# Kernel optimization log

Hardware: AMD Instinct MI355X
Metric: run time of the kernel (lower is better)

## Reference

```python
import jax, jax.numpy as jnp
import numpy as np

MIN_NORM = 1e-15
PROJ_EPS = 4e-3  # HGCN float32 boundary eps
C = 1.0          # curvature (all layers)
N_BRANCH = 4


def artanh(x):
    return jnp.arctanh(jnp.clip(x, -1.0 + 1e-7, 1.0 - 1e-7))


def _norm(x):
    return jnp.clip(jnp.linalg.norm(x, axis=-1, keepdims=True), MIN_NORM)


def proj(x, c):
    n = _norm(x)
    maxn = (1.0 - PROJ_EPS) / jnp.sqrt(c)
    return jnp.where(n > maxn, x / n * maxn, x)


def expmap0(u, c):
    sc = jnp.sqrt(c)
    n = _norm(u)
    return jnp.tanh(sc * n) * u / (sc * n)


def logmap0(p, c):
    sc = jnp.sqrt(c)
    n = _norm(p)
    return artanh(sc * n) * p / (sc * n)


def mobius_add(x, y, c):
    x2 = jnp.sum(x * x, -1, keepdims=True)
    y2 = jnp.sum(y * y, -1, keepdims=True)
    xy = jnp.sum(x * y, -1, keepdims=True)
    num = (1.0 + 2.0 * c * xy + c * y2) * x + (1.0 - c * x2) * y
    den = 1.0 + 2.0 * c * xy + c * c * x2 * y2
    return num / jnp.clip(den, MIN_NORM)


def mobius_matvec(W, x, c):
    sc = jnp.sqrt(c)
    xn = _norm(x)
    mx = x @ W.T
    mxn = _norm(mx)
    res = jnp.tanh(mxn / xn * artanh(sc * xn)) * mx / (mxn * sc)
    zero = jnp.all(mx == 0, axis=-1, keepdims=True)
    return jnp.where(zero, jnp.zeros((), x.dtype), res)


def mobius_mulscaler(r, x, c):
    sc = jnp.sqrt(c)
    xn = _norm(x)
    return jnp.tanh(r * artanh(sc * xn)) * x / (xn * sc)


def spmm(src, dst, w, xt, n):
    # out[i] = sum_{e: dst[e]=i} w[e] * xt[src[e]]
    return jax.ops.segment_sum(w[:, None] * xt[src], dst, num_segments=n)


def hgc_layer(h, W, b, src, dst, w, n):
    # HypLinear (dropout=0)
    h = proj(mobius_matvec(W, h, C), C)
    hb = proj(expmap0(b[None, :], C), C)
    h = proj(mobius_add(h, hb, C), C)
    # HypAgg: sparse propagation in tangent space
    st = spmm(src, dst, w, logmap0(h, C), n)
    h = proj(expmap0(st, C), C)
    # HypAct (relu)
    return proj(expmap0(jax.nn.relu(logmap0(h, C)), C), C)


def encode(x, W0, b0, W1, b1, src, dst, w, n):
    h = proj(expmap0(x, C), C)  # proj_tan0 is identity on Poincare ball
    h = hgc_layer(h, W0, b0, src, dst, w, n)
    h = hgc_layer(h, W1, b1, src, dst, w, n)
    return h


def setup_inputs() -> dict:
    key = jax.random.key(0)
    ks = jax.random.split(key, 8)
    N, F_IN, HID, DIM, E = 50000, 128, 128, 64, 1600000
    x = jax.random.normal(ks[0], (N, F_IN), jnp.float32)
    edge_src = jax.random.randint(ks[1], (E,), 0, N, jnp.int32)
    edge_dst = jax.random.randint(ks[2], (E,), 0, N, jnp.int32)
    # positive, roughly row-normalized edge weights (avg degree 32)
    edge_w = jax.random.uniform(ks[3], (N_BRANCH, E), jnp.float32) / 32.0
    W0 = jax.random.normal(ks[4], (N_BRANCH, HID, F_IN), jnp.float32) * 0.05
    b0 = jax.random.normal(ks[5], (N_BRANCH, HID), jnp.float32) * 0.01
    W1 = jax.random.normal(ks[6], (N_BRANCH, DIM, HID), jnp.float32) * 0.05
    b1 = jax.random.normal(ks[7], (N_BRANCH, DIM), jnp.float32) * 0.01
    return {"x": x, "edge_src": edge_src, "edge_dst": edge_dst, "edge_w": edge_w,
            "W0": W0, "b0": b0, "W1": W1, "b1": b1}


def reference(x, edge_src, edge_dst, edge_w, W0, b0, W1, b1):
    n = x.shape[0]
    # 4 directional-proximity branches (d_i, d_o, n_i, n_o); fixed small loop
    branches = [encode(x, W0[i], b0[i], W1[i], b1[i], edge_src, edge_dst, edge_w[i], n)
                for i in range(N_BRANCH)]
    # Mobius-weighted (scalar 1/8) combination, left-to-right mobius_add chain
    target = mobius_mulscaler(0.125, branches[0], C)
    for br in branches[1:]:
        target = mobius_add(target, mobius_mulscaler(0.125, br, C), C)
    feat = jnp.stack(branches + [target], axis=1)  # [N, 5, dim]
    # HypAttnAgg (use_att=False) with row-normalized per-node star adjacency:
    # target row of each 5-block = mean of the 5 tangent vectors
    agg = logmap0(feat, C).mean(axis=1)            # [N, dim]
    return proj(expmap0(agg, C), C)
```

## Files before the change

### kernel.cpp

```cpp
#include <hip/hip_runtime.h>
#include <math.h>

#define MAXN_P 0.996f

typedef unsigned short bfraw;
typedef __attribute__((ext_vector_type(8))) short bf16x8;
typedef __attribute__((ext_vector_type(4))) float f32x4;

__device__ __forceinline__ float wred(float v){
  #pragma unroll
  for(int o=32;o>0;o>>=1) v += __shfl_xor(v,o,64);
  return v;
}
template<int W>
__device__ __forceinline__ float gredw(float v){
  #pragma unroll
  for(int o=W/2;o>0;o>>=1) v += __shfl_xor(v,o,64);
  return v;
}
__device__ __forceinline__ float artanh_c(float x){
  x = fminf(fmaxf(x, -1.0f+1e-7f), 1.0f-1e-7f);
  return atanhf(x);
}
__device__ __forceinline__ float sel4(float4 w, int g){
  float ab = (g&1) ? w.y : w.x;
  float cd = (g&1) ? w.w : w.z;
  return (g&2) ? cd : ab;
}
__device__ __forceinline__ bfraw f2bf(float f){
  unsigned u = __float_as_uint(f);
  unsigned r = (u + 0x7fffu + ((u>>16)&1u)) >> 16;
  return (bfraw)r;
}
__device__ __forceinline__ float bflo(unsigned u){ return __uint_as_float(u<<16); }
__device__ __forceinline__ float bfhi(unsigned u){ return __uint_as_float(u & 0xffff0000u); }

__device__ __forceinline__ void acc8(float* a, float w, uint4 u){
  a[0]=fmaf(w, bflo(u.x), a[0]); a[1]=fmaf(w, bfhi(u.x), a[1]);
  a[2]=fmaf(w, bflo(u.y), a[2]); a[3]=fmaf(w, bfhi(u.y), a[3]);
  a[4]=fmaf(w, bflo(u.z), a[4]); a[5]=fmaf(w, bfhi(u.z), a[5]);
  a[6]=fmaf(w, bflo(u.w), a[6]); a[7]=fmaf(w, bfhi(u.w), a[7]);
}
__device__ __forceinline__ void acc4(float* a, float w, uint2 u){
  a[0]=fmaf(w, bflo(u.x), a[0]); a[1]=fmaf(w, bfhi(u.x), a[1]);
  a[2]=fmaf(w, bflo(u.y), a[2]); a[3]=fmaf(w, bfhi(u.y), a[3]);
}

template<int W, int K>
__device__ __forceinline__ float postK(const float* u, float* h){
  float ss = 0.f;
  #pragma unroll
  for(int k=0;k<K;k++) ss += u[k]*u[k];
  ss = gredw<W>(ss);
  float un = fmaxf(sqrtf(ss), 1e-15f);
  float t1 = tanhf(un);
  float sc = t1/un;
  float pn = t1;
  if (pn > MAXN_P){ sc *= MAXN_P/pn; pn = MAXN_P; }
  float ln = fmaxf(pn, 1e-15f);
  float m = sc * (artanh_c(ln)/ln);
  float v[K]; float vs = 0.f;
  #pragma unroll
  for(int k=0;k<K;k++){ v[k] = fmaxf(u[k]*m, 0.f); vs += v[k]*v[k]; }
  vs = gredw<W>(vs);
  float vn = fmaxf(sqrtf(vs), 1e-15f);
  float t2 = tanhf(vn);
  float qs = t2/vn;
  float qn = t2;
  if (qn > MAXN_P){ qs *= MAXN_P/qn; qn = MAXN_P; }
  #pragma unroll
  for(int k=0;k<K;k++) h[k] = v[k]*qs;
  return qn;
}

__global__ __launch_bounds__(256) void k_prologue(
    const float* __restrict__ x, bfraw* __restrict__ h0, float* __restrict__ n0, int N,
    const int* __restrict__ dst, int* __restrict__ cnt, int E,
    const float* __restrict__ W0, bfraw* __restrict__ w0b, int nW0,
    const float* __restrict__ W1, bfraw* __restrict__ w1b, int nW1,
    const float* __restrict__ b0, const float* __restrict__ b1,
    float* __restrict__ hb0, float* __restrict__ hb1, int HID, int DIM,
    int RB, int HIST, int W0B, int W1B)
{
  int b = blockIdx.x;
  int tid = threadIdx.x;
  if (b < RB){
    int wid = (b*256 + tid)>>6;
    int lane = tid & 63;
    if (wid >= N) return;
    const float* r = x + (size_t)wid*128;
    float u0 = r[lane], u1 = r[lane+64];
    float ss = wred(u0*u0 + u1*u1);
    float un = fmaxf(sqrtf(ss), 1e-15f);
    float tn = tanhf(un);
    float sc = tn/un;
    float pn = tn;
    if (pn > MAXN_P){ sc *= MAXN_P/pn; pn = MAXN_P; }
    h0[(size_t)wid*128 + lane]      = f2bf(u0*sc);
    h0[(size_t)wid*128 + lane + 64] = f2bf(u1*sc);
    if (lane == 0) n0[wid] = pn;
    return;
  }
  b -= RB;
  if (b < HIST){
    int e = b*256 + tid;
    if (e < E) atomicAdd(&cnt[dst[e]], 1);
    return;
  }
  b -= HIST;
  if (b < W0B){
    int i = b*256 + tid;
    if (i < nW0) w0b[i] = f2bf(W0[i]);
    return;
  }
  b -= W0B;
  if (b < W1B){
    int i = b*256 + tid;
    if (i < nW1) w1b[i] = f2bf(W1[i]);
    return;
  }
  b -= W1B;
  {
    if (tid >= 64) return;
    int layer = b >> 2, br = b & 3;
    int D = layer ? DIM : HID;
    const float* bb = layer ? (b1 + (size_t)br*DIM) : (b0 + (size_t)br*HID);
    float* o        = layer ? (hb1 + (size_t)br*DIM) : (hb0 + (size_t)br*HID);
    float v0 = (tid < D) ? bb[tid] : 0.f;
    float v1 = (tid+64 < D) ? bb[tid+64] : 0.f;
    float ss = wred(v0*v0 + v1*v1);
    float n = fmaxf(sqrtf(ss), 1e-15f);
    float tn = tanhf(n);
    float sc = tn/n;
    if (tn > MAXN_P) sc *= MAXN_P/tn;
    if (tid < D)    o[tid]    = v0*sc;
    if (tid+64 < D) o[tid+64] = v1*sc;
  }
}

__global__ __launch_bounds__(256) void k_scan1(const int* __restrict__ cnt, int* __restrict__ bsum, int N){
  __shared__ int sh[256];
  int base = blockIdx.x*2048;
  int tid = threadIdx.x;
  int loc = 0;
  #pragma unroll
  for(int j=0;j<8;j++){
    int i = base + tid*8 + j;
    loc += (i < N) ? cnt[i] : 0;
  }
  sh[tid] = loc;
  __syncthreads();
  for(int off=128; off>0; off>>=1){
    if (tid < off) sh[tid] += sh[tid+off];
    __syncthreads();
  }
  if (tid == 0) bsum[blockIdx.x] = sh[0];
}
__global__ void k_scan2(int* __restrict__ bsum, int nb){
  if (threadIdx.x == 0){
    int run = 0;
    for(int i=0;i<nb;i++){ int t = bsum[i]; bsum[i] = run; run += t; }
  }
}
__global__ __launch_bounds__(256) void k_scan3(const int* __restrict__ cnt, const int* __restrict__ bsum,
                                               int* __restrict__ rowptr, int* __restrict__ cursor, int N){
  __shared__ int sh[256];
  int base = blockIdx.x*2048;
  int tid = threadIdx.x;
  int v[8]; int loc = 0;
  #pragma unroll
  for(int j=0;j<8;j++){
    int i = base + tid*8 + j;
    v[j] = (i < N) ? cnt[i] : 0;
    loc += v[j];
  }
  sh[tid] = loc;
  __syncthreads();
  for(int off=1; off<256; off<<=1){
    int add = (tid>=off) ? sh[tid-off] : 0;
    __syncthreads();
    sh[tid] += add;
    __syncthreads();
  }
  int run = ((tid==0) ? 0 : sh[tid-1]) + bsum[blockIdx.x];
  #pragma unroll
  for(int j=0;j<8;j++){
    int i = base + tid*8 + j;
    if (i < N){
      rowptr[i] = run; cursor[i] = run; run += v[j];
      if (i == N-1) rowptr[N] = run;
    }
  }
}

__global__ void k_fill(const int* __restrict__ src, const int* __restrict__ dst,
                       const float* __restrict__ ew, int E,
                       int* __restrict__ cursor, int* __restrict__ srcs,
                       float4* __restrict__ wq){
  int e = blockIdx.x*blockDim.x + threadIdx.x;
  if (e >= E) return;
  int d = dst[e];
  int pos = atomicAdd(&cursor[d], 1);
  srcs[pos] = src[e];
  wq[pos] = make_float4(ew[e], ew[(size_t)E + e], ew[2*(size_t)E + e], ew[3*(size_t)E + e]);
}

template<int CT>
__global__ __launch_bounds__(256) void k_gemm_fused(
    const bfraw* __restrict__ Abase, int lda, int abroff,
    const bfraw* __restrict__ Wb,
    const float* __restrict__ nin, int nstride, int nbroff,
    const float* __restrict__ hball,
    bfraw* __restrict__ xt,
    int M)
{
  constexpr int BN = CT*16;
  __shared__ bfraw tile[64*BN];
  int br = blockIdx.z;
  const bfraw* A = Abase + (size_t)br*abroff;
  const bfraw* W = Wb + (size_t)br*BN*128;
  const float* hb = hball + (size_t)br*BN;
  int rb = blockIdx.x*64;
  int t = threadIdx.x;
  int wave = t>>6, lane = t&63;
  int cl = lane&15, grp = lane>>4;

  int rowA = rb + wave*16 + cl;
  bf16x8 afr[4];
  bf16x8 zf = {0,0,0,0,0,0,0,0};
  #pragma unroll
  for(int ks=0;ks<4;ks++){
    if (rowA < M) afr[ks] = *(const bf16x8*)(A + (size_t)rowA*lda + ks*32 + grp*8);
    else          afr[ks] = zf;
  }
  f32x4 acc[CT];
  #pragma unroll
  for(int ct=0;ct<CT;ct++) acc[ct] = f32x4{0.f,0.f,0.f,0.f};
  #pragma unroll
  for(int ct=0;ct<CT;ct++){
    #pragma unroll
    for(int ks=0;ks<4;ks++){
      bf16x8 bfr = *(const bf16x8*)(W + (size_t)(ct*16+cl)*128 + ks*32 + grp*8);
      acc[ct] = __builtin_amdgcn_mfma_f32_16x16x32_bf16(afr[ks], bfr, acc[ct], 0,0,0);
    }
  }
  float hv[CT]; float hb2 = 0.f;
  #pragma unroll
  for(int ct=0;ct<CT;ct++){ hv[ct] = hb[cl+16*ct]; hb2 += hv[ct]*hv[ct]; }
  hb2 = gredw<16>(hb2);
  #pragma unroll
  for(int j=0;j<4;j++){
    int rloc = wave*16 + grp*4 + j;
    int node = rb + rloc;
    bool v = node < M;
    float m[CT]; float ss = 0.f;
    #pragma unroll
    for(int ct=0;ct<CT;ct++){ m[ct] = acc[ct][j]; ss += m[ct]*m[ct]; }
    ss = gredw<16>(ss);
    float mxn_raw = sqrtf(ss);
    float mxn = fmaxf(mxn_raw, 1e-15f);
    float xn = fmaxf(v ? nin[(size_t)node*nstride + br*nbroff] : 1.f, 1e-15f);
    float th = tanhf(mxn/xn * artanh_c(xn));
    float hs = (mxn_raw > 0.f) ? th/mxn : 0.f;
    float hn = (mxn_raw > 0.f) ? th : 0.f;
    if (hn > MAXN_P){ hs *= MAXN_P/hn; hn = MAXN_P; }
    float h[CT]; float xy = 0.f, x2 = 0.f;
    #pragma unroll
    for(int ct=0;ct<CT;ct++){ h[ct] = m[ct]*hs; xy += h[ct]*hv[ct]; x2 += h[ct]*h[ct]; }
    xy = gredw<16>(xy); x2 = gredw<16>(x2);
    float c1 = 1.f + 2.f*xy + hb2;
    float c2 = 1.f - x2;
    float den = fmaxf(1.f + 2.f*xy + x2*hb2, 1e-15f);
    float a[CT]; float as = 0.f;
    #pragma unroll
    for(int ct=0;ct<CT;ct++){ a[ct] = (c1*h[ct] + c2*hv[ct])/den; as += a[ct]*a[ct]; }
    as = gredw<16>(as);
    float an = fmaxf(sqrtf(as), 1e-15f);
    float s2 = 1.f;
    if (an > MAXN_P){ s2 = MAXN_P/an; an = MAXN_P; }
    float ls = artanh_c(an)/an * s2;
    #pragma unroll
    for(int ct=0;ct<CT;ct++) tile[rloc*BN + cl + 16*ct] = f2bf(a[ct]*ls);
  }
  __syncthreads();
  constexpr int IT = (64*BN)/(256*8);
  #pragma unroll
  for(int i=0;i<IT;i++){
    int flat = (t + i*256)*8;
    int row = flat/BN, col = flat%BN;
    int node = rb + row;
    if (node < M)
      *(uint4*)(xt + ((size_t)node*4 + br)*BN + col) = *(const uint4*)(tile + row*BN + col);
  }
}

__global__ __launch_bounds__(256) void k_spmm_l0(const int* __restrict__ rowptr,
                        const int* __restrict__ srcs, const float4* __restrict__ wq,
                        const bfraw* __restrict__ xt,
                        bfraw* __restrict__ hout, float* __restrict__ n4, int N){
  int wid = (blockIdx.x*blockDim.x + threadIdx.x)>>6;
  int lane = threadIdx.x & 63;
  if (wid >= N) return;
  int g = lane>>4;
  float acc[8] = {0,0,0,0,0,0,0,0};
  int p0 = rowptr[wid], p1 = rowptr[wid+1];
  int p = p0;
  for (; p+8 <= p1; p += 8){
    int s[8]; float4 w[8]; uint4 u[8];
    #pragma unroll
    for(int i=0;i<8;i++){ s[i] = srcs[p+i]; w[i] = wq[p+i]; }
    #pragma unroll
    for(int i=0;i<8;i++) u[i] = *((const uint4*)(xt + (size_t)s[i]*512) + lane);
    #pragma unroll
    for(int i=0;i<8;i++) acc8(acc, sel4(w[i],g), u[i]);
  }
  for (; p+2 <= p1; p += 2){
    int s0 = srcs[p], s1 = srcs[p+1];
    float4 w0 = wq[p], w1 = wq[p+1];
    uint4 u0 = *((const uint4*)(xt + (size_t)s0*512) + lane);
    uint4 u1 = *((const uint4*)(xt + (size_t)s1*512) + lane);
    acc8(acc, sel4(w0,g), u0);
    acc8(acc, sel4(w1,g), u1);
  }
  if (p < p1){
    int s0 = srcs[p];
    float4 w0 = wq[p];
    uint4 u0 = *((const uint4*)(xt + (size_t)s0*512) + lane);
    acc8(acc, sel4(w0,g), u0);
  }
  float h[8];
  float qn = postK<16,8>(acc, h);
  uint4 o;
  o.x = (unsigned)f2bf(h[0]) | ((unsigned)f2bf(h[1])<<16);
  o.y = (unsigned)f2bf(h[2]) | ((unsigned)f2bf(h[3])<<16);
  o.z = (unsigned)f2bf(h[4]) | ((unsigned)f2bf(h[5])<<16);
  o.w = (unsigned)f2bf(h[6]) | ((unsigned)f2bf(h[7])<<16);
  *((uint4*)(hout + (size_t)wid*512) + lane) = o;
  if ((lane&15)==0) n4[(size_t)wid*4 + g] = qn;
}

__global__ __launch_bounds__(256) void k_spmm_l1(const int* __restrict__ rowptr,
                        const int* __restrict__ srcs, const float4* __restrict__ wq,
                        const bfraw* __restrict__ xt,
                        float* __restrict__ out, int N){
  int wid = (blockIdx.x*blockDim.x + threadIdx.x)>>6;
  int lane = threadIdx.x & 63;
  if (wid >= N) return;
  int g = lane>>4;
  int slot = lane & 15;
  float acc[4] = {0,0,0,0};
  int p0 = rowptr[wid], p1 = rowptr[wid+1];
  int p = p0;
  for (; p+8 <= p1; p += 8){
    int s[8]; float4 w[8]; uint2 u[8];
    #pragma unroll
    for(int i=0;i<8;i++){ s[i] = srcs[p+i]; w[i] = wq[p+i]; }
    #pragma unroll
    for(int i=0;i<8;i++) u[i] = *((const uint2*)(xt + (size_t)s[i]*256) + lane);
    #pragma unroll
    for(int i=0;i<8;i++) acc4(acc, sel4(w[i],g), u[i]);
  }
  for (; p+2 <= p1; p += 2){
    int s0 = srcs[p], s1 = srcs[p+1];
    float4 w0 = wq[p], w1 = wq[p+1];
    uint2 u0 = *((const uint2*)(xt + (size_t)s0*256) + lane);
    uint2 u1 = *((const uint2*)(xt + (size_t)s1*256) + lane);
    acc4(acc, sel4(w0,g), u0);
    acc4(acc, sel4(w1,g), u1);
  }
  if (p < p1){
    int s0 = srcs[p];
    float4 w0 = wq[p];
    uint2 u0 = *((const uint2*)(xt + (size_t)s0*256) + lane);
    acc4(acc, sel4(w0,g), u0);
  }
  float hv[4];
  float qn = postK<16,4>(acc, hv);
  float xk[4][4]; float qk[4];
  #pragma unroll
  for(int k=0;k<4;k++){
    #pragma unroll
    for(int j=0;j<4;j++) xk[k][j] = __shfl(hv[j], slot + 16*k, 64);
    qk[k] = __shfl(qn, 16*k, 64);
  }
  float xn0 = fmaxf(qk[0], 1e-15f);
  float s0 = tanhf(0.125f*artanh_c(xn0))/xn0;
  float t[4] = {s0*xk[0][0], s0*xk[0][1], s0*xk[0][2], s0*xk[0][3]};
  #pragma unroll
  for(int k=1;k<4;k++){
    float yn = fmaxf(qk[k], 1e-15f);
    float sy = tanhf(0.125f*artanh_c(yn))/yn;
    float y[4] = {sy*xk[k][0], sy*xk[k][1], sy*xk[k][2], sy*xk[k][3]};
    float dx=0.f, dy=0.f, dxy=0.f;
    #pragma unroll
    for(int j=0;j<4;j++){ dx += t[j]*t[j]; dy += y[j]*y[j]; dxy += t[j]*y[j]; }
    float x2 = gredw<16>(dx);
    float y2 = gredw<16>(dy);
    float xy = gredw<16>(dxy);
    float c1 = 1.f + 2.f*xy + y2;
    float c2 = 1.f - x2;
    float den = fmaxf(1.f + 2.f*xy + x2*y2, 1e-15f);
    #pragma unroll
    for(int j=0;j<4;j++) t[j] = (c1*t[j] + c2*y[j])/den;
  }
  float s[4] = {0,0,0,0};
  #pragma unroll
  for(int k=0;k<4;k++){
    float nk = fmaxf(qk[k], 1e-15f);
    float lk = artanh_c(nk)/nk;
    #pragma unroll
    for(int j=0;j<4;j++) s[j] = fmaf(lk, xk[k][j], s[j]);
  }
  float dt = 0.f;
  #pragma unroll
  for(int j=0;j<4;j++) dt += t[j]*t[j];
  float tn = fmaxf(sqrtf(gredw<16>(dt)), 1e-15f);
  float lt = artanh_c(tn)/tn;
  #pragma unroll
  for(int j=0;j<4;j++) s[j] = 0.2f*fmaf(lt, t[j], s[j]);
  float ds = 0.f;
  #pragma unroll
  for(int j=0;j<4;j++) ds += s[j]*s[j];
  float an = fmaxf(sqrtf(gredw<16>(ds)), 1e-15f);
  float on = tanhf(an);
  float osc = on/an;
  if (on > MAXN_P) osc *= MAXN_P/on;
  if (g == 0)
    *(float4*)(out + (size_t)wid*64 + 4*slot) =
      make_float4(s[0]*osc, s[1]*osc, s[2]*osc, s[3]*osc);
}

extern "C" void kernel_launch(void* const* d_in, const int* in_sizes, int n_in,
                              void* d_out, int out_size, void* d_ws, size_t ws_size,
                              hipStream_t stream){
  const float* x   = (const float*)d_in[0];
  const int*   src = (const int*)d_in[1];
  const int*   dst = (const int*)d_in[2];
  const float* ew  = (const float*)d_in[3];
  const float* W0  = (const float*)d_in[4];
  const float* b0  = (const float*)d_in[5];
  const float* W1  = (const float*)d_in[6];
  const float* b1  = (const float*)d_in[7];
  float* out = (float*)d_out;

  const int FIN = 128;
  int N = in_sizes[0]/FIN;
  int E = in_sizes[1];
  int HID = in_sizes[5]/4;
  int DIM = in_sizes[7]/4;

  char* ws = (char*)d_ws;
  size_t off = 0;
  auto alloc = [&](size_t bytes)->char*{
    char* p = ws + off;
    off += (bytes + 255) & ~(size_t)255;
    return p;
  };
  bfraw* h4b    = (bfraw*)alloc((size_t)N*4*FIN*2);
  bfraw* xtb    = (bfraw*)alloc((size_t)N*4*FIN*2);
  float* n0     = (float*)alloc((size_t)N*4);
  float* n4     = (float*)alloc((size_t)N*16);
  int*   rowptr = (int*)alloc((size_t)(N+1)*4);
  int*   cnt    = (int*)alloc((size_t)N*4);
  int*   cursor = (int*)alloc((size_t)N*4);
  int*   srcs   = (int*)alloc((size_t)E*4);
  float4* wq    = (float4*)alloc((size_t)E*16);
  float* hb0    = (float*)alloc((size_t)4*HID*4);
  float* hb1    = (float*)alloc((size_t)4*DIM*4);
  bfraw* w0b    = (bfraw*)alloc((size_t)4*HID*FIN*2);
  bfraw* w1b    = (bfraw*)alloc((size_t)4*DIM*HID*2);
  int*   bsum   = (int*)alloc((size_t)256*4);
  (void)ws_size; (void)n_in; (void)out_size;

  bfraw* h0 = h4b;

  int rowBlocks = (N + 3)/4;
  int nW0 = 4*HID*FIN, nW1 = 4*DIM*HID;
  int RB = rowBlocks;
  int HIST = (E + 255)/256;
  int W0B = (nW0 + 255)/256;
  int W1B = (nW1 + 255)/256;
  int nscan = (N + 2047)/2048;

  hipMemsetAsync(cnt, 0, (size_t)N*4, stream);
  k_prologue<<<RB + HIST + W0B + W1B + 8, 256, 0, stream>>>(
      x, h0, n0, N, dst, cnt, E, W0, w0b, nW0, W1, w1b, nW1,
      b0, b1, hb0, hb1, HID, DIM, RB, HIST, W0B, W1B);

  k_scan1<<<nscan, 256, 0, stream>>>(cnt, bsum, N);
  k_scan2<<<1, 64, 0, stream>>>(bsum, nscan);
  k_scan3<<<nscan, 256, 0, stream>>>(cnt, bsum, rowptr, cursor, N);
  k_fill<<<HIST, 256, 0, stream>>>(src, dst, ew, E, cursor, srcs, wq);

  k_gemm_fused<8><<<dim3((N+63)/64, 1, 4), 256, 0, stream>>>(
      h0, FIN, 0, w0b, n0, 1, 0, hb0, xtb, N);
  k_spmm_l0<<<rowBlocks, 256, 0, stream>>>(rowptr, srcs, wq, xtb, h4b, n4, N);

  k_gemm_fused<4><<<dim3((N+63)/64, 1, 4), 256, 0, stream>>>(
      h4b, 4*HID, HID, w1b, n4, 4, 1, hb1, xtb, N);
  k_spmm_l1<<<rowBlocks, 256, 0, stream>>>(rowptr, srcs, wq, xtb, out, N);
}
```

Measured before the change: 716.4 us.

## Process two rows per wavefront in layer-1 SpMM with wider loads

The layer-1 SpMM kernel now assigns two destination rows to each 64-lane wavefront, 32 lanes per row, with each lane loading 16-byte chunks (8 bf16) instead of 8-byte chunks. The edge loop runs to the maximum degree of the two rows and masks invalid edges with a zero weight. The per-branch norm and combination reductions move from 16-lane to 8-lane groups, and the launch uses half as many blocks. This aims for more memory parallelism and wider gathers, at the cost of lanes idling when the two rows' degrees differ and higher register use.

```diff
diff --git a/kernel.cpp b/kernel.cpp
--- a/kernel.cpp
+++ b/kernel.cpp
@@ -40,10 +40,6 @@
   a[2]=fmaf(w, bflo(u.y), a[2]); a[3]=fmaf(w, bfhi(u.y), a[3]);
   a[4]=fmaf(w, bflo(u.z), a[4]); a[5]=fmaf(w, bfhi(u.z), a[5]);
   a[6]=fmaf(w, bflo(u.w), a[6]); a[7]=fmaf(w, bfhi(u.w), a[7]);
-}
-__device__ __forceinline__ void acc4(float* a, float w, uint2 u){
-  a[0]=fmaf(w, bflo(u.x), a[0]); a[1]=fmaf(w, bfhi(u.x), a[1]);
-  a[2]=fmaf(w, bflo(u.y), a[2]); a[3]=fmaf(w, bfhi(u.y), a[3]);
 }
 
 template<int W, int K>
@@ -343,91 +339,94 @@
                         const int* __restrict__ srcs, const float4* __restrict__ wq,
                         const bfraw* __restrict__ xt,
                         float* __restrict__ out, int N){
-  int wid = (blockIdx.x*blockDim.x + threadIdx.x)>>6;
+  int wpair = (blockIdx.x*blockDim.x + threadIdx.x)>>6;
   int lane = threadIdx.x & 63;
-  if (wid >= N) return;
-  int g = lane>>4;
-  int slot = lane & 15;
-  float acc[4] = {0,0,0,0};
-  int p0 = rowptr[wid], p1 = rowptr[wid+1];
-  int p = p0;
-  for (; p+8 <= p1; p += 8){
-    int s[8]; float4 w[8]; uint2 u[8];
-    #pragma unroll
-    for(int i=0;i<8;i++){ s[i] = srcs[p+i]; w[i] = wq[p+i]; }
-    #pragma unroll
-    for(int i=0;i<8;i++) u[i] = *((const uint2*)(xt + (size_t)s[i]*256) + lane);
-    #pragma unroll
-    for(int i=0;i<8;i++) acc4(acc, sel4(w[i],g), u[i]);
-  }
-  for (; p+2 <= p1; p += 2){
-    int s0 = srcs[p], s1 = srcs[p+1];
-    float4 w0 = wq[p], w1 = wq[p+1];
-    uint2 u0 = *((const uint2*)(xt + (size_t)s0*256) + lane);
-    uint2 u1 = *((const uint2*)(xt + (size_t)s1*256) + lane);
-    acc4(acc, sel4(w0,g), u0);
-    acc4(acc, sel4(w1,g), u1);
-  }
-  if (p < p1){
-    int s0 = srcs[p];
-    float4 w0 = wq[p];
-    uint2 u0 = *((const uint2*)(xt + (size_t)s0*256) + lane);
-    acc4(acc, sel4(w0,g), u0);
-  }
-  float hv[4];
-  float qn = postK<16,4>(acc, hv);
-  float xk[4][4]; float qk[4];
-  #pragma unroll
-  for(int k=0;k<4;k++){
-    #pragma unroll
-    for(int j=0;j<4;j++) xk[k][j] = __shfl(hv[j], slot + 16*k, 64);
-    qk[k] = __shfl(qn, 16*k, 64);
-  }
-  float xn0 = fmaxf(qk[0], 1e-15f);
-  float s0 = tanhf(0.125f*artanh_c(xn0))/xn0;
-  float t[4] = {s0*xk[0][0], s0*xk[0][1], s0*xk[0][2], s0*xk[0][3]};
+  int half = lane>>5;
+  int l31 = lane & 31;
+  int row = wpair*2 + half;
+  bool rv = row < N;
+  int rc = rv ? row : 0;
+  int p0 = rowptr[rc];
+  int p1 = rv ? rowptr[rc+1] : p0;
+  int deg = p1 - p0;
+  int mx = deg;
+  #pragma unroll
+  for(int o=32;o>0;o>>=1) mx = max(mx, __shfl_xor(mx, o, 64));
+  int g = l31 >> 3;
+  int slot = l31 & 7;
+  float acc[8] = {0,0,0,0,0,0,0,0};
+  for (int i = 0; i < mx; i += 4){
+    int pe[4]; float wv[4]; uint4 u[4];
+    #pragma unroll
+    for(int j=0;j<4;j++){
+      int pi = p0 + i + j;
+      bool v = pi < p1;
+      pe[j] = v ? pi : 0;
+      wv[j] = v ? 1.f : 0.f;
+    }
+    int s[4]; float4 w4[4];
+    #pragma unroll
+    for(int j=0;j<4;j++){ s[j] = srcs[pe[j]]; w4[j] = wq[pe[j]]; }
+    #pragma unroll
+    for(int j=0;j<4;j++) u[j] = *((const uint4*)(xt + (size_t)s[j]*256) + l31);
+    #pragma unroll
+    for(int j=0;j<4;j++) acc8(acc, wv[j]*sel4(w4[j],g), u[j]);
+  }
+  float h[8];
+  float qn = postK<8,8>(acc, h);
+  int hb = half*32;
+  float t[8], s[8];
+  float qk0 = fmaxf(__shfl(qn, hb + 0, 64), 1e-15f);
+  float lk0 = artanh_c(qk0)/qk0;
+  float s0 = tanhf(0.125f*artanh_c(qk0))/qk0;
+  #pragma unroll
+  for(int j=0;j<8;j++){
+    float xv = __shfl(h[j], hb + slot, 64);
+    t[j] = s0*xv;
+    s[j] = lk0*xv;
+  }
   #pragma unroll
   for(int k=1;k<4;k++){
-    float yn = fmaxf(qk[k], 1e-15f);
-    float sy = tanhf(0.125f*artanh_c(yn))/yn;
-    float y[4] = {sy*xk[k][0], sy*xk[k][1], sy*xk[k][2], sy*xk[k][3]};
+    float qk = fmaxf(__shfl(qn, hb + k*8, 64), 1e-15f);
+    float lk = artanh_c(qk)/qk;
+    float sy = tanhf(0.125f*artanh_c(qk))/qk;
+    float y[8];
     float dx=0.f, dy=0.f, dxy=0.f;
     #pragma unroll
-    for(int j=0;j<4;j++){ dx += t[j]*t[j]; dy += y[j]*y[j]; dxy += t[j]*y[j]; }
-    float x2 = gredw<16>(dx);
-    float y2 = gredw<16>(dy);
-    float xy = gredw<16>(dxy);
+    for(int j=0;j<8;j++){
+      float xv = __shfl(h[j], hb + k*8 + slot, 64);
+      y[j] = sy*xv;
+      s[j] = fmaf(lk, xv, s[j]);
+      dx += t[j]*t[j]; dy += y[j]*y[j]; dxy += t[j]*y[j];
+    }
+    float x2 = gredw<8>(dx);
+    float y2 = gredw<8>(dy);
+    float xy = gredw<8>(dxy);
     float c1 = 1.f + 2.f*xy + y2;
     float c2 = 1.f - x2;
     float den = fmaxf(1.f + 2.f*xy + x2*y2, 1e-15f);
     #pragma unroll
-    for(int j=0;j<4;j++) t[j] = (c1*t[j] + c2*y[j])/den;
-  }
-  float s[4] = {0,0,0,0};
-  #pragma unroll
-  for(int k=0;k<4;k++){
-    float nk = fmaxf(qk[k], 1e-15f);
-    float lk = artanh_c(nk)/nk;
-    #pragma unroll
-    for(int j=0;j<4;j++) s[j] = fmaf(lk, xk[k][j], s[j]);
+    for(int j=0;j<8;j++) t[j] = (c1*t[j] + c2*y[j])/den;
   }
   float dt = 0.f;
   #pragma unroll
-  for(int j=0;j<4;j++) dt += t[j]*t[j];
-  float tn = fmaxf(sqrtf(gredw<16>(dt)), 1e-15f);
+  for(int j=0;j<8;j++) dt += t[j]*t[j];
+  float tn = fmaxf(sqrtf(gredw<8>(dt)), 1e-15f);
   float lt = artanh_c(tn)/tn;
   #pragma unroll
-  for(int j=0;j<4;j++) s[j] = 0.2f*fmaf(lt, t[j], s[j]);
+  for(int j=0;j<8;j++) s[j] = 0.2f*fmaf(lt, t[j], s[j]);
   float ds = 0.f;
   #pragma unroll
-  for(int j=0;j<4;j++) ds += s[j]*s[j];
-  float an = fmaxf(sqrtf(gredw<16>(ds)), 1e-15f);
+  for(int j=0;j<8;j++) ds += s[j]*s[j];
+  float an = fmaxf(sqrtf(gredw<8>(ds)), 1e-15f);
   float on = tanhf(an);
   float osc = on/an;
   if (on > MAXN_P) osc *= MAXN_P/on;
-  if (g == 0)
-    *(float4*)(out + (size_t)wid*64 + 4*slot) =
-      make_float4(s[0]*osc, s[1]*osc, s[2]*osc, s[3]*osc);
+  if (g == 0 && rv){
+    float* orow = out + (size_t)row*64 + slot*8;
+    *(float4*)(orow)     = make_float4(s[0]*osc, s[1]*osc, s[2]*osc, s[3]*osc);
+    *(float4*)(orow + 4) = make_float4(s[4]*osc, s[5]*osc, s[6]*osc, s[7]*osc);
+  }
 }
 
 extern "C" void kernel_launch(void* const* d_in, const int* in_sizes, int n_in,
@@ -475,6 +474,7 @@
   bfraw* h0 = h4b;
 
   int rowBlocks = (N + 3)/4;
+  int pairBlocks = (N + 7)/8;
   int nW0 = 4*HID*FIN, nW1 = 4*DIM*HID;
   int RB = rowBlocks;
   int HIST = (E + 255)/256;
@@ -498,5 +498,5 @@
 
   k_gemm_fused<4><<<dim3((N+63)/64, 1, 4), 256, 0, stream>>>(
       h4b, 4*HID, HID, w1b, n4, 4, 1, hb1, xtb, N);
-  k_spmm_l1<<<rowBlocks, 256, 0, stream>>>(rowptr, srcs, wq, xtb, out, N);
-}
+  k_spmm_l1<<<pairBlocks, 256, 0, stream>>>(rowptr, srcs, wq, xtb, out, N);
+}
```

Measured after the change: 677.0 us. 1.06x faster.
